# Kernel optimization log

Hardware: AMD Instinct MI355X
Metric: run time of the kernel (lower is better)

The kernel has to match this reference:

```python
import jax, jax.numpy as jnp
from jax import lax
import numpy as np

N_TOTAL = 262144
NUM_SAMPLE = 1024
KNN_K = 16
NUM_CLASSES = 13
HIDDEN = 128
EPS = 1e-8


def _sqdist(a, b):
    # (Na,3),(Nb,3) -> (Na,Nb) squared euclidean; same argmin as torch.cdist
    return (jnp.sum(a * a, axis=1)[:, None]
            + jnp.sum(b * b, axis=1)[None, :]
            - 2.0 * a @ b.T)


def _farthest_point_sample(xyz, n_samples):
    # sequential FPS starting from index 0 (deterministic start)
    n = xyz.shape[0]

    def step(carry, _):
        min_d2, last = carry
        d2 = jnp.sum((xyz - xyz[last]) ** 2, axis=-1)
        min_d2 = jnp.minimum(min_d2, d2)
        nxt = jnp.argmax(min_d2).astype(jnp.int32)
        return (min_d2, nxt), nxt

    init = (jnp.full((n,), 1e10, dtype=xyz.dtype), jnp.int32(0))
    _, idxs = lax.scan(step, init, None, length=n_samples - 1)
    return jnp.concatenate([jnp.zeros((1,), jnp.int32), idxs])


def _compute_normals(pts, k):
    # PCA normal per point from its k nearest neighbors (self excluded)
    d2 = _sqdist(pts, pts)                      # (S,S), S=1024 -> small
    _, nbr_idx = lax.top_k(-d2, k + 1)
    nbr = pts[nbr_idx[:, 1:]]                   # (S,k,3)
    centered = nbr - jnp.mean(nbr, axis=1, keepdims=True)
    cov = jnp.einsum('ski,skj->sij', centered, centered) / (k - 1)
    _, eigvecs = jnp.linalg.eigh(cov)           # ascending eigenvalues
    normal = eigvecs[..., 0]                    # smallest-eigval eigenvector
    return normal / (jnp.linalg.norm(normal, axis=-1, keepdims=True) + EPS)


def _forward(gaussian_positions, gaussian_colors, W1, b1, W2, b2, W3, b3):
    sample_idx = _farthest_point_sample(gaussian_positions, NUM_SAMPLE)
    dxyz = gaussian_positions[sample_idx]       # (S,3)
    drgb = gaussian_colors[sample_idx]          # (S,3)
    dnrm = _compute_normals(dxyz, KNN_K)        # (S,3)
    feats = jnp.concatenate([dxyz, drgb, dnrm], axis=1)  # (S,9)

    # pointwise segmentation network (stand-in for PointNet++ get_model)
    h = jax.nn.relu(feats @ W1 + b1)
    h = jax.nn.relu(h @ W2 + b2)
    pred = h @ W3 + b3                          # (S, num_classes)

    feat_down = jax.nn.softmax(pred, axis=1)
    lbl_down = jnp.argmax(pred, axis=1)

    # 1-NN label propagation: streaming-min candidate (memory-bound)
    d2_full = _sqdist(gaussian_positions, dxyz)  # (N, S) ~ 1 GB
    nearest = jnp.argmin(d2_full, axis=1)
    return feat_down[nearest], lbl_down[nearest]


def setup_inputs() -> dict:
    key = jax.random.key(0)
    ks = jax.random.split(key, 8)
    pos = jax.random.normal(ks[0], (N_TOTAL, 3), jnp.float32)
    col = jax.random.uniform(ks[1], (N_TOTAL, 3), jnp.float32)
    W1 = jax.random.normal(ks[2], (9, HIDDEN), jnp.float32) / np.sqrt(9.0)
    b1 = jnp.zeros((HIDDEN,), jnp.float32)
    W2 = jax.random.normal(ks[3], (HIDDEN, HIDDEN), jnp.float32) / np.sqrt(HIDDEN)
    b2 = jnp.zeros((HIDDEN,), jnp.float32)
    W3 = jax.random.normal(ks[4], (HIDDEN, NUM_CLASSES), jnp.float32) / np.sqrt(HIDDEN)
    b3 = jnp.zeros((NUM_CLASSES,), jnp.float32)
    return {"gaussian_positions": pos, "gaussian_colors": col,
            "W1": W1, "b1": b1, "W2": W2, "b2": b2, "W3": W3, "b3": b3}


def reference(gaussian_positions, gaussian_colors, W1, b1, W2, b2, W3, b3):
    return _forward(gaussian_positions, gaussian_colors, W1, b1, W2, b2, W3, b3)
```

## Files before the change

kernel.cpp:

```cpp
#include <hip/hip_runtime.h>
#include <math.h>

#define N_TOTAL    262144
#define NUM_SAMPLE 1024
#define FPS_BLOCKS 64
#define FPS_THREADS 256
#define FPS_PPT (N_TOTAL / (FPS_BLOCKS * FPS_THREADS))
#define M_WAVE 8
#define POOL (FPS_BLOCKS * 4 * M_WAVE)
#define ENT_PER_T (POOL / FPS_THREADS)
#define SEL_CAP 1023

__device__ __forceinline__ float addrn(float a, float b) { return __fadd_rn(a, b); }
__device__ __forceinline__ float subrn(float a, float b) { return __fsub_rn(a, b); }
__device__ __forceinline__ float mulrn(float a, float b) { return __fmul_rn(a, b); }

__device__ __forceinline__ float d2rn(float ax, float ay, float az,
                                      float bx, float by, float bz) {
  float dx = subrn(ax, bx), dy = subrn(ay, by), dz = subrn(az, bz);
  return addrn(addrn(mulrn(dx, dx), mulrn(dy, dy)), mulrn(dz, dz));
}

template <int CTRL>
__device__ __forceinline__ int dpp_i(int x) {
  return __builtin_amdgcn_update_dpp(x, x, CTRL, 0xF, 0xF, false);
}
__device__ __forceinline__ float wave_fmax_bcast(float v) {
  v = fmaxf(v, __int_as_float(dpp_i<0x111>(__float_as_int(v))));
  v = fmaxf(v, __int_as_float(dpp_i<0x112>(__float_as_int(v))));
  v = fmaxf(v, __int_as_float(dpp_i<0x114>(__float_as_int(v))));
  v = fmaxf(v, __int_as_float(dpp_i<0x118>(__float_as_int(v))));
  v = fmaxf(v, __int_as_float(dpp_i<0x142>(__float_as_int(v))));
  v = fmaxf(v, __int_as_float(dpp_i<0x143>(__float_as_int(v))));
  return __int_as_float(__builtin_amdgcn_readlane(__float_as_int(v), 63));
}
__device__ __forceinline__ unsigned wave_umax_bcast(unsigned v) {
  unsigned o;
  o = (unsigned)dpp_i<0x111>((int)v); v = (o > v) ? o : v;
  o = (unsigned)dpp_i<0x112>((int)v); v = (o > v) ? o : v;
  o = (unsigned)dpp_i<0x114>((int)v); v = (o > v) ? o : v;
  o = (unsigned)dpp_i<0x118>((int)v); v = (o > v) ? o : v;
  o = (unsigned)dpp_i<0x142>((int)v); v = (o > v) ? o : v;
  o = (unsigned)dpp_i<0x143>((int)v); v = (o > v) ? o : v;
  return (unsigned)__builtin_amdgcn_readlane((int)v, 63);
}

__device__ __forceinline__ float slapy2f(float x, float y) {
  float xa = fabsf(x), ya = fabsf(y);
  float w = fmaxf(xa, ya), z = fminf(xa, ya);
  if (z == 0.f) return w;
  float t = z / w;
  return w * __fsqrt_rn(1.f + t * t);
}

__device__ __forceinline__ void slartgf(float f, float g, float& c, float& s, float& r) {
  if (g == 0.f) { c = 1.f; s = 0.f; r = f; }
  else if (f == 0.f) { c = 0.f; s = (g > 0.f) ? 1.f : -1.f; r = fabsf(g); }
  else {
    float d = __fsqrt_rn(f * f + g * g);
    c = fabsf(f) / d;
    r = (f >= 0.f) ? d : -d;
    s = g / r;
  }
}

__device__ void slaev2f(float a, float b, float c0, float& rt1, float& rt2,
                        float& cs1, float& sn1) {
  float sm = a + c0, df = a - c0;
  float adf = fabsf(df), tb = b + b, ab = fabsf(tb);
  float acmx, acmn;
  if (fabsf(a) > fabsf(c0)) { acmx = a; acmn = c0; } else { acmx = c0; acmn = a; }
  float rt;
  if (adf > ab)      { float t = ab / adf; rt = adf * __fsqrt_rn(1.f + t * t); }
  else if (adf < ab) { float t = adf / ab; rt = ab * __fsqrt_rn(1.f + t * t); }
  else               { rt = ab * __fsqrt_rn(2.f); }
  int sgn1;
  if (sm < 0.f)      { rt1 = 0.5f * (sm - rt); sgn1 = -1; rt2 = (acmx / rt1) * acmn - (b / rt1) * b; }
  else if (sm > 0.f) { rt1 = 0.5f * (sm + rt); sgn1 = 1;  rt2 = (acmx / rt1) * acmn - (b / rt1) * b; }
  else               { rt1 = 0.5f * rt; rt2 = -0.5f * rt; sgn1 = 1; }
  float cs; int sgn2;
  if (df >= 0.f) { cs = df + rt; sgn2 = 1; } else { cs = df - rt; sgn2 = -1; }
  float acs = fabsf(cs);
  if (acs > ab) {
    float ct = -tb / cs;
    sn1 = 1.f / __fsqrt_rn(1.f + ct * ct);
    cs1 = ct * sn1;
  } else {
    if (ab == 0.f) { cs1 = 1.f; sn1 = 0.f; }
    else { float tn = -cs / tb; cs1 = 1.f / __fsqrt_rn(1.f + tn * tn); sn1 = tn * cs1; }
  }
  if (sgn1 == sgn2) { float tn = cs1; cs1 = -sn1; sn1 = tn; }
}

#define D_(i) d[(i)-1]
#define E_(i) e[(i)-1]

__device__ void ssteqr3(float d[3], float e[2], float Z[3][3]) {
  const float eps    = 5.9604645e-08f;
  const float eps2   = 3.5527137e-15f;
  const float safmin = 1.17549435e-38f;
  const float ssfmax = 3.0744573e+18f;
  const float ssfmin = 3.0517578e-05f;
  const int n = 3;
  int jtot = 0, nmaxit = 90;
  int l1 = 1;

  while (true) {
    if (l1 > n) break;
    if (l1 > 1) E_(l1 - 1) = 0.f;
    int m = n;
    for (int mm = l1; mm <= n - 1; ++mm) {
      float tst = fabsf(E_(mm));
      if (tst == 0.f) { m = mm; break; }
      if (tst <= (__fsqrt_rn(fabsf(D_(mm))) * __fsqrt_rn(fabsf(D_(mm + 1)))) * eps) {
        E_(mm) = 0.f; m = mm; break;
      }
    }
    int l = l1, lsv = l, lend = m, lendsv = m;
    l1 = m + 1;
    if (lend == l) continue;

    float anorm = fabsf(D_(lend));
    for (int i2 = l; i2 <= lend - 1; ++i2) {
      anorm = fmaxf(anorm, fabsf(D_(i2)));
      anorm = fmaxf(anorm, fabsf(E_(i2)));
    }
    int iscale = 0;
    if (anorm == 0.f) continue;
    if (anorm > ssfmax) {
      iscale = 1; float mul = ssfmax / anorm;
      for (int i2 = l; i2 <= lend; ++i2) D_(i2) *= mul;
      for (int i2 = l; i2 <= lend - 1; ++i2) E_(i2) *= mul;
    } else if (anorm < ssfmin) {
      iscale = 2; float mul = ssfmin / anorm;
      for (int i2 = l; i2 <= lend; ++i2) D_(i2) *= mul;
      for (int i2 = l; i2 <= lend - 1; ++i2) E_(i2) *= mul;
    }

    if (fabsf(D_(lend)) < fabsf(D_(l))) { int t = l; l = lend; lend = t; }

    if (lend > l) {
      while (true) {
        int m2 = lend;
        if (l != lend) {
          for (int mm = l; mm <= lend - 1; ++mm) {
            float tst = fabsf(E_(mm)); tst = tst * tst;
            if (tst <= (eps2 * fabsf(D_(mm))) * fabsf(D_(mm + 1)) + safmin) { m2 = mm; break; }
          }
        }
        if (m2 < lend) E_(m2) = 0.f;
        float p = D_(l);
        if (m2 == l) { D_(l) = p; l = l + 1; if (l <= lend) continue; break; }
        if (m2 == l + 1) {
          float rt1, rt2, cc, ss;
          slaev2f(D_(l), E_(l), D_(l + 1), rt1, rt2, cc, ss);
          for (int i2 = 0; i2 < 3; ++i2) {
            float tmp = Z[i2][l];
            Z[i2][l]     = cc * tmp - ss * Z[i2][l - 1];
            Z[i2][l - 1] = ss * tmp + cc * Z[i2][l - 1];
          }
          D_(l) = rt1; D_(l + 1) = rt2; E_(l) = 0.f;
          l = l + 2; if (l <= lend) continue; break;
        }
        if (jtot == nmaxit) break;
        ++jtot;
        float g = (D_(l + 1) - p) / (2.f * E_(l));
        float r = slapy2f(g, 1.f);
        float sgn_rg = (g >= 0.f) ? r : -r;
        g = D_(m2) - p + E_(l) / (g + sgn_rg);
        float s = 1.f, c = 1.f;
        p = 0.f;
        float csv[2], ssv[2];
        for (int i2 = m2 - 1; i2 >= l; --i2) {
          float f = s * E_(i2);
          float b = c * E_(i2);
          slartgf(g, f, c, s, r);
          if (i2 != m2 - 1) E_(i2 + 1) = r;
          g = D_(i2 + 1) - p;
          r = (D_(i2) - g) * s + 2.f * c * b;
          p = s * r;
          D_(i2 + 1) = g + p;
          g = c * r - b;
          csv[i2 - l] = c; ssv[i2 - l] = -s;
        }
        for (int j = m2 - 1; j >= l; --j) {
          float ct = csv[j - l], st = ssv[j - l];
          for (int i2 = 0; i2 < 3; ++i2) {
            float tmp = Z[i2][j];
            Z[i2][j]     = ct * tmp - st * Z[i2][j - 1];
            Z[i2][j - 1] = st * tmp + ct * Z[i2][j - 1];
          }
        }
        D_(l) = D_(l) - p;
        E_(l) = g;
      }
    } else {
      while (true) {
        int m2 = lend;
        if (l != lend) {
          for (int mm = l; mm >= lend + 1; --mm) {
            float tst = fabsf(E_(mm - 1)); tst = tst * tst;
            if (tst <= (eps2 * fabsf(D_(mm))) * fabsf(D_(mm - 1)) + safmin) { m2 = mm; break; }
          }
        }
        if (m2 > lend) E_(m2 - 1) = 0.f;
        float p = D_(l);
        if (m2 == l) { D_(l) = p; l = l - 1; if (l >= lend) continue; break; }
        if (m2 == l - 1) {
          float rt1, rt2, cc, ss;
          slaev2f(D_(l - 1), E_(l - 1), D_(l), rt1, rt2, cc, ss);
          for (int i2 = 0; i2 < 3; ++i2) {
            float tmp = Z[i2][l - 1];
            Z[i2][l - 1] = cc * tmp - ss * Z[i2][l - 2];
            Z[i2][l - 2] = ss * tmp + cc * Z[i2][l - 2];
          }
          D_(l - 1) = rt1; D_(l) = rt2; E_(l - 1) = 0.f;
          l = l - 2; if (l >= lend) continue; break;
        }
        if (jtot == nmaxit) break;
        ++jtot;
        float g = (D_(l - 1) - p) / (2.f * E_(l - 1));
        float r = slapy2f(g, 1.f);
        float sgn_rg = (g >= 0.f) ? r : -r;
        g = D_(m2) - p + E_(l - 1) / (g + sgn_rg);
        float s = 1.f, c = 1.f;
        p = 0.f;
        float csv[2], ssv[2];
        for (int i2 = m2; i2 <= l - 1; ++i2) {
          float f = s * E_(i2);
          float b = c * E_(i2);
          slartgf(g, f, c, s, r);
          if (i2 != m2) E_(i2 - 1) = r;
          g = D_(i2) - p;
          r = (D_(i2 + 1) - g) * s + 2.f * c * b;
          p = s * r;
          D_(i2) = g + p;
          g = c * r - b;
          csv[i2 - m2] = c; ssv[i2 - m2] = s;
        }
        for (int j = m2; j <= l - 1; ++j) {
          float ct = csv[j - m2], st = ssv[j - m2];
          for (int i2 = 0; i2 < 3; ++i2) {
            float tmp = Z[i2][j];
            Z[i2][j]     = ct * tmp - st * Z[i2][j - 1];
            Z[i2][j - 1] = st * tmp + ct * Z[i2][j - 1];
          }
        }
        D_(l) = D_(l) - p;
        E_(l - 1) = g;
      }
    }
    if (iscale == 1) {
      float mul = anorm / ssfmax;
      for (int i2 = lsv; i2 <= lendsv; ++i2) D_(i2) *= mul;
      for (int i2 = lsv; i2 <= lendsv - 1; ++i2) E_(i2) *= mul;
    } else if (iscale == 2) {
      float mul = anorm / ssfmin;
      for (int i2 = lsv; i2 <= lendsv; ++i2) D_(i2) *= mul;
      for (int i2 = lsv; i2 <= lendsv - 1; ++i2) E_(i2) *= mul;
    }
  }
  for (int ii = 2; ii <= n; ++ii) {
    int i2 = ii - 1, k = i2;
    float p = D_(i2);
    for (int j = ii; j <= n; ++j) if (D_(j) < p) { k = j; p = D_(j); }
    if (k != i2) {
      D_(k) = D_(i2); D_(i2) = p;
      for (int rr = 0; rr < 3; ++rr) {
        float t = Z[rr][i2 - 1]; Z[rr][i2 - 1] = Z[rr][k - 1]; Z[rr][k - 1] = t;
      }
    }
  }
}

__device__ void eigh3_smallest(float a00, float a10, float a20, float a11, float a21, float a22,
                               float& nx, float& ny, float& nz) {
  float d[3], e[2];
  float Z[3][3] = {{1.f,0.f,0.f},{0.f,1.f,0.f},{0.f,0.f,1.f}};
  float tau, v2;
  {
    float alpha = a10, x = a20;
    float xnorm = fabsf(x);
    if (xnorm == 0.f) {
      tau = 0.f; v2 = 0.f;
      d[0] = a00; d[1] = a11; d[2] = a22;
      e[0] = alpha; e[1] = a21;
    } else {
      float beta = -copysignf(slapy2f(alpha, x), alpha);
      tau = (beta - alpha) / beta;
      v2 = x / (alpha - beta);
      float w0 = (tau * a11) + tau * (a21 * v2);
      float w1 = (tau * a21) + (tau * v2) * a22;
      float ac = (-0.5f * tau) * (w0 + w1 * v2);
      w0 = w0 + ac;
      w1 = w1 + ac * v2;
      d[0] = a00;
      d[1] = (a11 - w0) - w0;
      d[2] = (a22 - v2 * w1) - w1 * v2;
      e[0] = beta;
      e[1] = (a21 - v2 * w0) - w1;
    }
  }
  ssteqr3(d, e, Z);
  if (tau != 0.f) {
    for (int c = 0; c < 3; ++c) {
      float w = Z[1][c] + Z[2][c] * v2;
      float temp = (-tau) * w;
      Z[1][c] = Z[1][c] + temp;
      Z[2][c] = Z[2][c] + v2 * temp;
    }
  }
  nx = Z[0][0]; ny = Z[1][0]; nz = Z[2][0];
}

__global__ void k0_init(unsigned long long* cand, int* sample_idx) {
  int t = blockIdx.x * blockDim.x + threadIdx.x;
  if (t < 2 * POOL) cand[t] = 0ull;
  if (t == 0) sample_idx[0] = 0;
}

__global__ __launch_bounds__(FPS_THREADS) void k1_fps(
    const float* __restrict__ pos,
    unsigned long long* __restrict__ cand,
    int* __restrict__ sample_idx) {
  __shared__ float sel_x[SEL_CAP], sel_y[SEL_CAP], sel_z[SEL_CAP];
  __shared__ float wb_md[2][4], wb_x[2][4], wb_y[2][4], wb_z[2][4];
  __shared__ unsigned wb_idf[2][4];
  __shared__ float tred_md[4];
  __shared__ unsigned tred_idf[4];
  __shared__ int sh_selcnt;

  const int tidx = threadIdx.x;
  const int lane = tidx & 63, wv = tidx >> 6;
  const int gtid = blockIdx.x * FPS_THREADS + tidx;

  float px[FPS_PPT], py[FPS_PPT], pz[FPS_PPT], md[FPS_PPT];
#pragma unroll
  for (int k = 0; k < FPS_PPT; ++k) {
    int p = gtid + k * (FPS_BLOCKS * FPS_THREADS);
    px[k] = pos[3 * p]; py[k] = pos[3 * p + 1]; pz[k] = pos[3 * p + 2];
    md[k] = 1e10f;
  }
  const unsigned idf0 = 0x3FFFFFu - (unsigned)gtid;
  if (tidx == 0) { sel_x[0] = pos[0]; sel_y[0] = pos[1]; sel_z[0] = pos[2]; }
  __syncthreads();
  int sel_cnt = 1, total = 0, bt = 0;
  while (total < NUM_SAMPLE - 1) {
    ++bt;
    for (int s = 0; s < sel_cnt; ++s) {
      float lx = sel_x[s], ly = sel_y[s], lz = sel_z[s];
#pragma unroll
      for (int k = 0; k < FPS_PPT; ++k)
        md[k] = fminf(md[k], d2rn(px[k], py[k], pz[k], lx, ly, lz));
    }
    const unsigned tag = (unsigned)bt & 1023u;
    unsigned long long* setbase = cand + (size_t)(bt & 1) * POOL;
    {
      float wmd[FPS_PPT];
#pragma unroll
      for (int k = 0; k < FPS_PPT; ++k) wmd[k] = md[k];
      unsigned long long mypub = 0ull;
      for (int r = 0; r < M_WAVE; ++r) {
        float bm = wmd[0]; unsigned bidf = idf0;
#pragma unroll
        for (int k = 1; k < FPS_PPT; ++k) {
          unsigned idfk = idf0 - ((unsigned)k << 14);
          if (wmd[k] > bm || (wmd[k] == bm && idfk > bidf)) { bm = wmd[k]; bidf = idfk; }
        }
        float wmx = wave_fmax_bcast(bm);
        unsigned tb = (bm == wmx) ? bidf : 0u;
        unsigned widf = wave_umax_bcast(tb);
        if (lane == r)
          mypub = ((unsigned long long)__float_as_uint(wmx) << 32) |
                  ((unsigned long long)widf << 10);
#pragma unroll
        for (int k = 0; k < FPS_PPT; ++k) {
          unsigned idfk = idf0 - ((unsigned)k << 14);
          if (wmd[k] == wmx && idfk == widf) wmd[k] = -1.f;
        }
      }
      if (lane < M_WAVE)
        __hip_atomic_store(setbase + blockIdx.x * (4 * M_WAVE) + wv * M_WAVE + lane,
                           mypub | tag, __ATOMIC_RELAXED, __HIP_MEMORY_SCOPE_AGENT);
    }
    const int base_w = tidx * ENT_PER_T;
    float cmd[ENT_PER_T]; unsigned cidf[ENT_PER_T];
    {
      unsigned done = 0;
      while (done != 0xFFu) {
#pragma unroll
        for (int j = 0; j < ENT_PER_T; ++j) {
          if (!((done >> j) & 1u)) {
            unsigned long long v = __hip_atomic_load(setbase + base_w + j,
                                                     __ATOMIC_RELAXED, __HIP_MEMORY_SCOPE_AGENT);
            if ((unsigned)(v & 1023ull) == tag) {
              done |= 1u << j;
              cmd[j] = __uint_as_float((unsigned)(v >> 32));
              cidf[j] = (unsigned)((v >> 10) & 0x3FFFFFull);
            }
          }
        }
        if (done != 0xFFu) __builtin_amdgcn_s_sleep(1);
      }
    }
    float cx[ENT_PER_T], cy[ENT_PER_T], cz[ENT_PER_T];
#pragma unroll
    for (int j = 0; j < ENT_PER_T; ++j) {
      int gidx = 0x3FFFFF - (int)cidf[j];
      cx[j] = pos[3 * gidx]; cy[j] = pos[3 * gidx + 1]; cz[j] = pos[3 * gidx + 2];
    }
    {
      float t7 = cmd[ENT_PER_T - 1]; unsigned t7i = cidf[ENT_PER_T - 1];
      float twm = wave_fmax_bcast(t7);
      unsigned ttb = (t7 == twm) ? t7i : 0u;
      unsigned twi = wave_umax_bcast(ttb);
      if (lane == 0) { tred_md[wv] = twm; tred_idf[wv] = twi; }
    }
    __syncthreads();
    float Tmd = tred_md[0]; unsigned Tidf = tred_idf[0];
#pragma unroll
    for (int w = 1; w < 4; ++w) {
      float m2 = tred_md[w]; unsigned i2v = tred_idf[w];
      if (m2 > Tmd || (m2 == Tmd && i2v > Tidf)) { Tmd = m2; Tidf = i2v; }
    }
    int picks = 0;
    const int room = (NUM_SAMPLE - 1) - total;
    for (;;) {
      const int q = picks & 1;
      float bm = cmd[0]; unsigned bidf = cidf[0]; int bj = 0;
#pragma unroll
      for (int j = 1; j < ENT_PER_T; ++j)
        if (cmd[j] > bm || (cmd[j] == bm && cidf[j] > bidf)) { bm = cmd[j]; bidf = cidf[j]; bj = j; }
      float wmx = wave_fmax_bcast(bm);
      unsigned tb = (bm == wmx) ? bidf : 0u;
      unsigned widf = wave_umax_bcast(tb);
      if (bm == wmx && bidf == widf) {
        wb_md[q][wv] = wmx; wb_idf[q][wv] = widf;
        wb_x[q][wv] = cx[bj]; wb_y[q][wv] = cy[bj]; wb_z[q][wv] = cz[bj];
      }
      __syncthreads();
      float gm = wb_md[q][0]; unsigned gi = wb_idf[q][0]; int gw = 0;
#pragma unroll
      for (int w = 1; w < 4; ++w) {
        float m2 = wb_md[q][w]; unsigned i2v = wb_idf[q][w];
        if (m2 > gm || (m2 == gm && i2v > gi)) { gm = m2; gi = i2v; gw = w; }
      }
      if ((gm < Tmd || (gm == Tmd && gi < Tidf)) || picks >= room) break;
      float Xp = wb_x[q][gw], Yp = wb_y[q][gw], Zp = wb_z[q][gw];
      if (tidx == 0) {
        sel_x[picks] = Xp; sel_y[picks] = Yp; sel_z[picks] = Zp;
        if (blockIdx.x == 0) sample_idx[1 + total + picks] = 0x3FFFFF - (int)gi;
      }
#pragma unroll
      for (int j = 0; j < ENT_PER_T; ++j) {
        if (cmd[j] == gm && cidf[j] == gi) cmd[j] = -1.f;
        float d2 = d2rn(cx[j], cy[j], cz[j], Xp, Yp, Zp);
        if (d2 < cmd[j]) cmd[j] = d2;
      }
      ++picks;
    }
    if (tidx == 0) sh_selcnt = picks;
    __syncthreads();
    sel_cnt = sh_selcnt;
    total += sel_cnt;
  }
}

__global__ __launch_bounds__(256) void k2a_knn(
    const float* __restrict__ pos, const float* __restrict__ col,
    const int* __restrict__ sample_idx,
    float4* __restrict__ sp4g, float* __restrict__ feats9) {
  __shared__ float4 sp[NUM_SAMPLE];
  const int tid = threadIdx.x, lane = tid & 63, wv = tid >> 6;
  for (int i = tid; i < NUM_SAMPLE; i += 256) {
    int idx = sample_idx[i];
    float x = pos[3 * idx], y = pos[3 * idx + 1], z = pos[3 * idx + 2];
    float nrm = addrn(addrn(mulrn(x, x), mulrn(y, y)), mulrn(z, z));
    float4 v = make_float4(x, y, z, nrm);
    sp[i] = v;
    if (blockIdx.x == 0) sp4g[i] = v;
  }
  __syncthreads();
  for (int it = 0; it < 4; ++it) {
    const int r = blockIdx.x * 16 + wv * 4 + it;
    float4 pr = sp[r];
    unsigned long long kk[16];
#pragma unroll
    for (int k = 0; k < 16; ++k) {
      int j = lane + 64 * k;
      float4 q = sp[j];
      float dot = fmaf(pr.z, q.z, fmaf(pr.y, q.y, mulrn(pr.x, q.x)));
      float d2 = subrn(addrn(pr.w, q.w), mulrn(2.f, dot));
      unsigned b = __float_as_uint(d2);
      unsigned sbits = (b & 0x80000000u) ? ~b : (b | 0x80000000u);
      kk[k] = ((unsigned long long)sbits << 32) | (unsigned)j;
    }
    int bi[17];
#pragma unroll
    for (int rsel = 0; rsel < 17; ++rsel) {
      unsigned long long best = 0xFFFFFFFFFFFFFFFFull;
#pragma unroll
      for (int k = 0; k < 16; ++k) best = (kk[k] < best) ? kk[k] : best;
#pragma unroll
      for (int mk = 1; mk < 64; mk <<= 1) {
        unsigned long long o = (unsigned long long)__shfl_xor((long long)best, mk, 64);
        best = (o < best) ? o : best;
      }
      int j = (int)(best & 0xFFFFFFFFull);
      bi[rsel] = j;
#pragma unroll
      for (int k = 0; k < 16; ++k)
        if (((j >> 6) == k) && ((j & 63) == lane)) kk[k] = 0xFFFFFFFFFFFFFFFFull;
    }
    float mx = 0.f, my = 0.f, mz = 0.f;
#pragma unroll
    for (int k = 1; k <= 16; ++k) {
      float4 q = sp[bi[k]];
      mx = addrn(mx, q.x); my = addrn(my, q.y); mz = addrn(mz, q.z);
    }
    mx = mulrn(mx, 0.0625f); my = mulrn(my, 0.0625f); mz = mulrn(mz, 0.0625f);
    float c00 = 0.f, c01 = 0.f, c02 = 0.f, c11 = 0.f, c12 = 0.f, c22 = 0.f;
#pragma unroll
    for (int k = 1; k <= 16; ++k) {
      float4 q = sp[bi[k]];
      float dx = subrn(q.x, mx), dy = subrn(q.y, my), dz = subrn(q.z, mz);
      c00 = addrn(c00, mulrn(dx, dx)); c01 = addrn(c01, mulrn(dx, dy));
      c02 = addrn(c02, mulrn(dx, dz)); c11 = addrn(c11, mulrn(dy, dy));
      c12 = addrn(c12, mulrn(dy, dz)); c22 = addrn(c22, mulrn(dz, dz));
    }
    c00 /= 15.f; c01 /= 15.f; c02 /= 15.f; c11 /= 15.f; c12 /= 15.f; c22 /= 15.f;

    float n0, n1, n2;
    eigh3_smallest(c00, c01, c02, c11, c12, c22, n0, n1, n2);
    float nn = __fsqrt_rn(addrn(addrn(mulrn(n0, n0), mulrn(n1, n1)), mulrn(n2, n2)));
    float den = addrn(nn, 1e-8f);
    n0 /= den; n1 /= den; n2 /= den;

    if (lane == 0) {
      int myidx = sample_idx[r];
      float* f = feats9 + r * 9;
      f[0] = pr.x; f[1] = pr.y; f[2] = pr.z;
      f[3] = col[3 * myidx]; f[4] = col[3 * myidx + 1]; f[5] = col[3 * myidx + 2];
      f[6] = n0; f[7] = n1; f[8] = n2;
    }
  }
}

__global__ __launch_bounds__(64) void k2b_mlp(
    const float* __restrict__ W1, const float* __restrict__ b1,
    const float* __restrict__ W2, const float* __restrict__ b2,
    const float* __restrict__ W3, const float* __restrict__ b3,
    const float* __restrict__ feats9,
    float* __restrict__ featd, int* __restrict__ lbl) {
  __shared__ float hbuf[64][129];
  const int tid = threadIdx.x;
  const int r = blockIdx.x * 64 + tid;
  float f9[9];
#pragma unroll
  for (int k = 0; k < 9; ++k) f9[k] = feats9[r * 9 + k];
  for (int jo = 0; jo < 128; ++jo) {
    float acc = 0.f;
#pragma unroll
    for (int k = 0; k < 9; ++k) acc = fmaf(f9[k], W1[k * 128 + jo], acc);
    acc += b1[jo];
    hbuf[tid][jo] = fmaxf(acc, 0.f);
  }
  float pd[13];
#pragma unroll
  for (int c = 0; c < 13; ++c) pd[c] = 0.f;
  for (int io = 0; io < 128; io += 16) {
    float acc[16];
#pragma unroll
    for (int t = 0; t < 16; ++t) acc[t] = 0.f;
    for (int j = 0; j < 128; ++j) {
      float hj = hbuf[tid][j];
#pragma unroll
      for (int t = 0; t < 16; ++t) acc[t] = fmaf(hj, W2[j * 128 + io + t], acc[t]);
    }
#pragma unroll
    for (int t = 0; t < 16; ++t) {
      float h2 = fmaxf(acc[t] + b2[io + t], 0.f);
#pragma unroll
      for (int c = 0; c < 13; ++c) pd[c] = fmaf(h2, W3[(io + t) * 13 + c], pd[c]);
    }
  }
#pragma unroll
  for (int c = 0; c < 13; ++c) pd[c] += b3[c];
  float mmax = pd[0];
#pragma unroll
  for (int c = 1; c < 13; ++c) mmax = fmaxf(mmax, pd[c]);
  float es = 0.f, ev[13];
#pragma unroll
  for (int c = 0; c < 13; ++c) { ev[c] = expf(pd[c] - mmax); es += ev[c]; }
#pragma unroll
  for (int c = 0; c < 13; ++c) featd[r * 13 + c] = ev[c] / es;
  int am = 0; float bv = pd[0];
#pragma unroll
  for (int c = 1; c < 13; ++c) { if (pd[c] > bv) { bv = pd[c]; am = c; } }
  lbl[r] = am;
}

__global__ __launch_bounds__(256) void k3_assign(
    const float* __restrict__ pos,
    const float4* __restrict__ sp4g,
    const float* __restrict__ featd,
    const int* __restrict__ lbl,
    float* __restrict__ out) {
  __shared__ float4 sp[NUM_SAMPLE];
  for (int i = threadIdx.x; i < NUM_SAMPLE; i += 256) sp[i] = sp4g[i];
  __syncthreads();
  int i = blockIdx.x * 256 + threadIdx.x;
  float x = pos[3 * i], y = pos[3 * i + 1], z = pos[3 * i + 2];
  float an = addrn(addrn(mulrn(x, x), mulrn(y, y)), mulrn(z, z));
  float bestd = 3.402823466e+38f; int bestj = 0;
#pragma unroll 4
  for (int j = 0; j < NUM_SAMPLE; ++j) {
    float4 q = sp[j];
    float dot = fmaf(z, q.z, fmaf(y, q.y, mulrn(x, q.x)));
    float d2 = subrn(addrn(an, q.w), mulrn(2.f, dot));
    if (d2 < bestd) { bestd = d2; bestj = j; }
  }
  const float* fr = featd + bestj * 13;
  float* o = out + (size_t)i * 13;
#pragma unroll
  for (int c = 0; c < 13; ++c) o[c] = fr[c];
  out[(size_t)N_TOTAL * 13 + i] = (float)lbl[bestj];
}

extern "C" void kernel_launch(void* const* d_in, const int* in_sizes, int n_in,
                              void* d_out, int out_size, void* d_ws, size_t ws_size,
                              hipStream_t stream) {
  (void)in_sizes; (void)n_in; (void)out_size; (void)ws_size;
  const float* pos = (const float*)d_in[0];
  const float* col = (const float*)d_in[1];
  const float* W1 = (const float*)d_in[2];
  const float* b1 = (const float*)d_in[3];
  const float* W2 = (const float*)d_in[4];
  const float* b2 = (const float*)d_in[5];
  const float* W3 = (const float*)d_in[6];
  const float* b3 = (const float*)d_in[7];
  float* out = (float*)d_out;

  char* w = (char*)d_ws;
  unsigned long long* cand = (unsigned long long*)(w);
  int* sample_idx = (int*)(w + 65536);
  float4* sp4g = (float4*)(w + 73728);
  float* featd = (float*)(w + 90112);
  int* lbl = (int*)(w + 143360);
  float* feats9 = (float*)(w + 147456);

  k0_init<<<16, 256, 0, stream>>>(cand, sample_idx);
  k1_fps<<<FPS_BLOCKS, FPS_THREADS, 0, stream>>>(pos, cand, sample_idx);
  k2a_knn<<<64, 256, 0, stream>>>(pos, col, sample_idx, sp4g, feats9);
  k2b_mlp<<<16, 64, 0, stream>>>(W1, b1, W2, b2, W3, b3, feats9, featd, lbl);
  k3_assign<<<N_TOTAL / 256, 256, 0, stream>>>(pos, sp4g, featd, lbl, out);
}
```

Measured before the change: 1.931 ms.

## Run FPS candidate selection in a single wave with packed 64-bit keys

The per-round candidate pool is staged into shared memory, and the sequential pick loop now runs on one wavefront instead of all four. This removes the per-pick __syncthreads and the cross-wave shared-memory reduction. Each lane holds four times as many candidates. Max-reductions now use a single packed 64-bit (distance bits, index) key via DPP instead of separate float and index reductions. The trade-off is more serial work per lane and idle waves during selection, in exchange for no block barriers inside the loop.

Result: slower. 2.948 ms (+52.7%).

```diff
diff --git a/kernel.cpp b/kernel.cpp
--- a/kernel.cpp
+++ b/kernel.cpp
@@ -9,6 +9,7 @@
 #define M_WAVE 8
 #define POOL (FPS_BLOCKS * 4 * M_WAVE)
 #define ENT_PER_T (POOL / FPS_THREADS)
+#define CPL (POOL / 64)
 #define SEL_CAP 1023
 
 __device__ __forceinline__ float addrn(float a, float b) { return __fadd_rn(a, b); }
@@ -25,14 +26,24 @@
 __device__ __forceinline__ int dpp_i(int x) {
   return __builtin_amdgcn_update_dpp(x, x, CTRL, 0xF, 0xF, false);
 }
-__device__ __forceinline__ float wave_fmax_bcast(float v) {
-  v = fmaxf(v, __int_as_float(dpp_i<0x111>(__float_as_int(v))));
-  v = fmaxf(v, __int_as_float(dpp_i<0x112>(__float_as_int(v))));
-  v = fmaxf(v, __int_as_float(dpp_i<0x114>(__float_as_int(v))));
-  v = fmaxf(v, __int_as_float(dpp_i<0x118>(__float_as_int(v))));
-  v = fmaxf(v, __int_as_float(dpp_i<0x142>(__float_as_int(v))));
-  v = fmaxf(v, __int_as_float(dpp_i<0x143>(__float_as_int(v))));
-  return __int_as_float(__builtin_amdgcn_readlane(__float_as_int(v), 63));
+template <int CTRL>
+__device__ __forceinline__ unsigned long long dpp_u64(unsigned long long v) {
+  unsigned lo = (unsigned)v, hi = (unsigned)(v >> 32);
+  unsigned olo = (unsigned)dpp_i<CTRL>((int)lo);
+  unsigned ohi = (unsigned)dpp_i<CTRL>((int)hi);
+  return ((unsigned long long)ohi << 32) | olo;
+}
+__device__ __forceinline__ unsigned long long wave_u64max_bcast(unsigned long long v) {
+  unsigned long long o;
+  o = dpp_u64<0x111>(v); if (o > v) v = o;
+  o = dpp_u64<0x112>(v); if (o > v) v = o;
+  o = dpp_u64<0x114>(v); if (o > v) v = o;
+  o = dpp_u64<0x118>(v); if (o > v) v = o;
+  o = dpp_u64<0x142>(v); if (o > v) v = o;
+  o = dpp_u64<0x143>(v); if (o > v) v = o;
+  unsigned lo = (unsigned)__builtin_amdgcn_readlane((int)(unsigned)v, 63);
+  unsigned hi = (unsigned)__builtin_amdgcn_readlane((int)(unsigned)(v >> 32), 63);
+  return ((unsigned long long)hi << 32) | lo;
 }
 __device__ __forceinline__ unsigned wave_umax_bcast(unsigned v) {
   unsigned o;
@@ -323,11 +334,9 @@
     const float* __restrict__ pos,
     unsigned long long* __restrict__ cand,
     int* __restrict__ sample_idx) {
+  __shared__ unsigned long long keyl[POOL];
+  __shared__ float pxl[POOL], pyl[POOL], pzl[POOL];
   __shared__ float sel_x[SEL_CAP], sel_y[SEL_CAP], sel_z[SEL_CAP];
-  __shared__ float wb_md[2][4], wb_x[2][4], wb_y[2][4], wb_z[2][4];
-  __shared__ unsigned wb_idf[2][4];
-  __shared__ float tred_md[4];
-  __shared__ unsigned tred_idf[4];
   __shared__ int sh_selcnt;
 
   const int tidx = threadIdx.x;
@@ -361,31 +370,32 @@
       for (int k = 0; k < FPS_PPT; ++k) wmd[k] = md[k];
       unsigned long long mypub = 0ull;
       for (int r = 0; r < M_WAVE; ++r) {
-        float bm = wmd[0]; unsigned bidf = idf0;
+        float bm = wmd[0]; unsigned bf = idf0;
 #pragma unroll
         for (int k = 1; k < FPS_PPT; ++k) {
           unsigned idfk = idf0 - ((unsigned)k << 14);
-          if (wmd[k] > bm || (wmd[k] == bm && idfk > bidf)) { bm = wmd[k]; bidf = idfk; }
-        }
-        float wmx = wave_fmax_bcast(bm);
-        unsigned tb = (bm == wmx) ? bidf : 0u;
-        unsigned widf = wave_umax_bcast(tb);
+          bool t = (wmd[k] > bm) || (wmd[k] == bm && idfk > bf);
+          if (t) { bm = wmd[k]; bf = idfk; }
+        }
+        unsigned long long kk = (bm < 0.f) ? 0ull
+            : (((unsigned long long)__float_as_uint(bm) << 32) | bf);
+        unsigned long long kw = wave_u64max_bcast(kk);
         if (lane == r)
-          mypub = ((unsigned long long)__float_as_uint(wmx) << 32) |
-                  ((unsigned long long)widf << 10);
+          mypub = (kw & 0xFFFFFFFF00000000ull) | ((kw & 0x3FFFFFull) << 10);
+        unsigned wmbits = (unsigned)(kw >> 32);
+        unsigned widf = (unsigned)(kw & 0x3FFFFFull);
 #pragma unroll
         for (int k = 0; k < FPS_PPT; ++k) {
           unsigned idfk = idf0 - ((unsigned)k << 14);
-          if (wmd[k] == wmx && idfk == widf) wmd[k] = -1.f;
+          if (__float_as_uint(wmd[k]) == wmbits && idfk == widf) wmd[k] = -1.f;
         }
       }
       if (lane < M_WAVE)
         __hip_atomic_store(setbase + blockIdx.x * (4 * M_WAVE) + wv * M_WAVE + lane,
                            mypub | tag, __ATOMIC_RELAXED, __HIP_MEMORY_SCOPE_AGENT);
     }
-    const int base_w = tidx * ENT_PER_T;
-    float cmd[ENT_PER_T]; unsigned cidf[ENT_PER_T];
     {
+      const int base_w = tidx * ENT_PER_T;
       unsigned done = 0;
       while (done != 0xFFu) {
 #pragma unroll
@@ -395,71 +405,75 @@
                                                      __ATOMIC_RELAXED, __HIP_MEMORY_SCOPE_AGENT);
             if ((unsigned)(v & 1023ull) == tag) {
               done |= 1u << j;
-              cmd[j] = __uint_as_float((unsigned)(v >> 32));
-              cidf[j] = (unsigned)((v >> 10) & 0x3FFFFFull);
+              unsigned long long vv = v & ~1023ull;
+              keyl[base_w + j] = vv;
+              int gidx = 0x3FFFFF - (int)((vv >> 10) & 0x3FFFFFull);
+              pxl[base_w + j] = pos[3 * gidx];
+              pyl[base_w + j] = pos[3 * gidx + 1];
+              pzl[base_w + j] = pos[3 * gidx + 2];
             }
           }
         }
         if (done != 0xFFu) __builtin_amdgcn_s_sleep(1);
       }
     }
-    float cx[ENT_PER_T], cy[ENT_PER_T], cz[ENT_PER_T];
-#pragma unroll
-    for (int j = 0; j < ENT_PER_T; ++j) {
-      int gidx = 0x3FFFFF - (int)cidf[j];
-      cx[j] = pos[3 * gidx]; cy[j] = pos[3 * gidx + 1]; cz[j] = pos[3 * gidx + 2];
-    }
-    {
-      float t7 = cmd[ENT_PER_T - 1]; unsigned t7i = cidf[ENT_PER_T - 1];
-      float twm = wave_fmax_bcast(t7);
-      unsigned ttb = (t7 == twm) ? t7i : 0u;
-      unsigned twi = wave_umax_bcast(ttb);
-      if (lane == 0) { tred_md[wv] = twm; tred_idf[wv] = twi; }
-    }
     __syncthreads();
-    float Tmd = tred_md[0]; unsigned Tidf = tred_idf[0];
-#pragma unroll
-    for (int w = 1; w < 4; ++w) {
-      float m2 = tred_md[w]; unsigned i2v = tred_idf[w];
-      if (m2 > Tmd || (m2 == Tmd && i2v > Tidf)) { Tmd = m2; Tidf = i2v; }
-    }
-    int picks = 0;
-    const int room = (NUM_SAMPLE - 1) - total;
-    for (;;) {
-      const int q = picks & 1;
-      float bm = cmd[0]; unsigned bidf = cidf[0]; int bj = 0;
-#pragma unroll
-      for (int j = 1; j < ENT_PER_T; ++j)
-        if (cmd[j] > bm || (cmd[j] == bm && cidf[j] > bidf)) { bm = cmd[j]; bidf = cidf[j]; bj = j; }
-      float wmx = wave_fmax_bcast(bm);
-      unsigned tb = (bm == wmx) ? bidf : 0u;
-      unsigned widf = wave_umax_bcast(tb);
-      if (bm == wmx && bidf == widf) {
-        wb_md[q][wv] = wmx; wb_idf[q][wv] = widf;
-        wb_x[q][wv] = cx[bj]; wb_y[q][wv] = cy[bj]; wb_z[q][wv] = cz[bj];
-      }
-      __syncthreads();
-      float gm = wb_md[q][0]; unsigned gi = wb_idf[q][0]; int gw = 0;
-#pragma unroll
-      for (int w = 1; w < 4; ++w) {
-        float m2 = wb_md[q][w]; unsigned i2v = wb_idf[q][w];
-        if (m2 > gm || (m2 == gm && i2v > gi)) { gm = m2; gi = i2v; gw = w; }
-      }
-      if ((gm < Tmd || (gm == Tmd && gi < Tidf)) || picks >= room) break;
-      float Xp = wb_x[q][gw], Yp = wb_y[q][gw], Zp = wb_z[q][gw];
-      if (tidx == 0) {
-        sel_x[picks] = Xp; sel_y[picks] = Yp; sel_z[picks] = Zp;
-        if (blockIdx.x == 0) sample_idx[1 + total + picks] = 0x3FFFFF - (int)gi;
-      }
-#pragma unroll
-      for (int j = 0; j < ENT_PER_T; ++j) {
-        if (cmd[j] == gm && cidf[j] == gi) cmd[j] = -1.f;
-        float d2 = d2rn(cx[j], cy[j], cz[j], Xp, Yp, Zp);
-        if (d2 < cmd[j]) cmd[j] = d2;
-      }
-      ++picks;
-    }
-    if (tidx == 0) sh_selcnt = picks;
+    if (wv == 0) {
+      float cmd[CPL]; unsigned cidf[CPL];
+      float cx[CPL], cy[CPL], cz[CPL];
+#pragma unroll
+      for (int j = 0; j < CPL; ++j) {
+        int e = j * 64 + lane;
+        unsigned long long v = keyl[e];
+        cmd[j] = __uint_as_float((unsigned)(v >> 32));
+        cidf[j] = (unsigned)((v >> 10) & 0x3FFFFFull);
+        cx[j] = pxl[e]; cy[j] = pyl[e]; cz[j] = pzl[e];
+      }
+      unsigned long long Tkey;
+      {
+        unsigned long long tk = 0ull;
+        if ((lane & 7) == 7) {
+          float bm = cmd[0]; unsigned bf = cidf[0];
+#pragma unroll
+          for (int j = 1; j < CPL; ++j) {
+            bool t = (cmd[j] > bm) || (cmd[j] == bm && cidf[j] > bf);
+            if (t) { bm = cmd[j]; bf = cidf[j]; }
+          }
+          tk = ((unsigned long long)__float_as_uint(bm) << 32) | bf;
+        }
+        Tkey = wave_u64max_bcast(tk);
+      }
+      int picks = 0;
+      const int room = (NUM_SAMPLE - 1) - total;
+      for (;;) {
+        float bm = cmd[0]; unsigned bf = cidf[0]; int bj = 0;
+#pragma unroll
+        for (int j = 1; j < CPL; ++j) {
+          bool t = (cmd[j] > bm) || (cmd[j] == bm && cidf[j] > bf);
+          if (t) { bm = cmd[j]; bf = cidf[j]; bj = j; }
+        }
+        unsigned long long mykey = (bm < 0.f) ? 0ull
+            : (((unsigned long long)__float_as_uint(bm) << 32) | bf);
+        unsigned long long keyWin = wave_u64max_bcast(mykey);
+        if (keyWin < Tkey || picks >= room) break;
+        unsigned ew = wave_umax_bcast((mykey == keyWin)
+                                      ? (unsigned)(bj * 64 + lane + 1) : 0u) - 1u;
+        float Xp = pxl[ew], Yp = pyl[ew], Zp = pzl[ew];
+        unsigned gidf = (unsigned)(keyWin & 0x3FFFFFull);
+        if (lane == 0) {
+          sel_x[picks] = Xp; sel_y[picks] = Yp; sel_z[picks] = Zp;
+          if (blockIdx.x == 0) sample_idx[1 + total + picks] = 0x3FFFFF - (int)gidf;
+        }
+#pragma unroll
+        for (int j = 0; j < CPL; ++j) {
+          float d2 = d2rn(cx[j], cy[j], cz[j], Xp, Yp, Zp);
+          float nm = fminf(cmd[j], d2);
+          cmd[j] = (cidf[j] == gidf) ? -1.f : nm;
+        }
+        ++picks;
+      }
+      if (lane == 0) sh_selcnt = picks;
+    }
     __syncthreads();
     sel_cnt = sh_selcnt;
     total += sel_cnt;
```
